# Kernel tuning notes

Hardware: AMD Instinct MI355X
Metric: run time of the kernel (lower is better)

Reference implementation:

```python
import jax, jax.numpy as jnp
import numpy as np
import math


def _neighbor_stack(x):
    # x: [b, nc, w, d] -> [b, nc, 3, w, d] with zero-padded prev/next chunks
    prev = jnp.pad(x[:, :-1], ((0, 0), (1, 0), (0, 0), (0, 0)))
    nxt = jnp.pad(x[:, 1:], ((0, 0), (0, 1), (0, 0), (0, 0)))
    return jnp.stack([prev, x, nxt], axis=2)


def local_attention(q, kv, Wq, Wkv, Wo, w):
    b, L, d_model = q.shape
    d_head = Wkv.shape[1] // 2
    h = d_model // d_head
    nc = L // w

    qp = (q @ Wq).reshape(b, L, h, d_head) / math.sqrt(d_head)
    kvp = kv @ Wkv  # [b, L, 2*d_head], single shared KV head (MQA)
    k, v = kvp[..., :d_head], kvp[..., d_head:]

    cq = qp.reshape(b, nc, w, h, d_head)
    k3 = _neighbor_stack(k.reshape(b, nc, w, d_head))  # [b, nc, 3, w, d]
    v3 = _neighbor_stack(v.reshape(b, nc, w, d_head))  # [b, nc, 3, w, d]

    # scores over (prev, self, next) chunks; padded edge chunks contribute
    # zero scores (exp(0)=1 in softmax), exactly as the torch F.pad(value=0) does.
    scores = jnp.einsum('bcxhd,bcpyd->bcxhpy', cq, k3)  # [b,nc,w,h,3,w]
    probs = jax.nn.softmax(scores.reshape(b, nc, w, h, 3 * w), axis=-1)
    probs = probs.reshape(b, nc, w, h, 3, w)

    ctx = jnp.einsum('bcxhpy,bcpyd->bcxhd', probs, v3)  # [b,nc,w,h,d]
    ctx = ctx.reshape(b, L, d_model)
    return ctx @ Wo


def setup_inputs() -> dict:
    key = jax.random.key(0)
    k1, k2, k3, k4, k5 = jax.random.split(key, 5)
    b, L, d_model, n_head = 1, 4096, 1024, 16
    d_head = d_model // n_head
    scale = 0.02
    return {
        'q': jax.random.normal(k1, (b, L, d_model), dtype=jnp.float32),
        'kv': jax.random.normal(k2, (b, L, d_model), dtype=jnp.float32),
        'Wq': jax.random.normal(k3, (d_model, d_model), dtype=jnp.float32) * scale,
        'Wkv': jax.random.normal(k4, (d_model, 2 * d_head), dtype=jnp.float32) * scale,
        'Wo': jax.random.normal(k5, (d_model, d_model), dtype=jnp.float32) * scale,
        'w': 512,
    }


def reference(q, kv, Wq, Wkv, Wo, w):
    return local_attention(q, kv, Wq, Wkv, Wo, w)
```

## Files before the change

kernel.cpp:

```cpp
#include <hip/hip_runtime.h>
#include <hip/hip_bf16.h>

typedef unsigned short u16;
typedef unsigned int u32;
typedef __attribute__((ext_vector_type(8))) short bf16x8;
typedef __attribute__((ext_vector_type(4))) float f32x4;
typedef __attribute__((ext_vector_type(16))) float f32x16;
typedef __attribute__((ext_vector_type(4))) u32 u32x4;

__device__ __forceinline__ u16 f2bf(float x) {
  __hip_bfloat16 h = __float2bfloat16(x);
  return __builtin_bit_cast(u16, h);
}

__device__ __forceinline__ u32 cvtpk(float lo, float hi) {
  u32 d;
  asm("v_cvt_pk_bf16_f32 %0, %1, %2" : "=v"(d) : "v"(lo), "v"(hi));
  return d;
}

#if __has_builtin(__builtin_amdgcn_exp2f)
#define EXP2(x) __builtin_amdgcn_exp2f(x)
#else
#define EXP2(x) __expf((x) * 0.6931471805599453f)
#endif

__device__ __forceinline__ bf16x8 mk_frag(u32 a, u32 b, u32 c, u32 d) {
  u32x4 v = {a, b, c, d};
  return __builtin_bit_cast(bf16x8, v);
}

__device__ __forceinline__ f32x16 mfma32(bf16x8 a, bf16x8 b, f32x16 c) {
  return __builtin_amdgcn_mfma_f32_32x32x16_bf16(a, b, c, 0, 0, 0);
}

__device__ __forceinline__ void gload16(const void* g, void* lds) {
  __builtin_amdgcn_global_load_lds((const __attribute__((address_space(1))) void*)g,
                                   (__attribute__((address_space(3))) void*)lds, 16, 0, 0);
}

__device__ __forceinline__ int xcd_swz(int bid, int cpx) {
  return (bid & 7) * cpx + (bid >> 3);
}

__global__ __launch_bounds__(256) void cvt_tw(const float* __restrict__ q, const float* __restrict__ kv,
                                              const float* __restrict__ Wq, const float* __restrict__ Wkv,
                                              const float* __restrict__ Wo, u16* __restrict__ qkbf,
                                              u16* __restrict__ wqt, u16* __restrict__ wkvt,
                                              u16* __restrict__ wot) {
  __shared__ float T[64][65];
  const int t = threadIdx.x;
  const int bid = blockIdx.x;
  if (bid < 4096) {
    int idx = bid * 256 + t;
    const float* src = (idx < 524288) ? q : kv;
    int li = idx & 524287;
    const float4* p = (const float4*)src + (size_t)li * 2;
    float4 a = p[0], b = p[1];
    bf16x8 vv;
    vv[0] = (short)f2bf(a.x); vv[1] = (short)f2bf(a.y);
    vv[2] = (short)f2bf(a.z); vv[3] = (short)f2bf(a.w);
    vv[4] = (short)f2bf(b.x); vv[5] = (short)f2bf(b.y);
    vv[6] = (short)f2bf(b.z); vv[7] = (short)f2bf(b.w);
    *(bf16x8*)(qkbf + (size_t)idx * 8) = vv;
    return;
  }
  const int wb = bid - 4096;
  const float* W; u16* Wt; int N, bx, by;
  if (wb < 256)      { W = Wq;  Wt = wqt;  N = 1024; bx = wb & 15; by = wb >> 4; }
  else if (wb < 512) { int b = wb - 256; W = Wo;  Wt = wot;  N = 1024; bx = b & 15; by = b >> 4; }
  else               { int b = wb - 512; W = Wkv; Wt = wkvt; N = 128;  bx = b & 1;  by = b >> 1; }
  const int K = 1024;
  const int n0 = bx * 64, k0 = by * 64;
  #pragma unroll
  for (int pass = 0; pass < 4; ++pass) {
    int r = pass * 16 + (t >> 4);
    int c = (t & 15) * 4;
    float4 v = *(const float4*)(W + (size_t)(k0 + r) * N + n0 + c);
    T[r][c] = v.x; T[r][c + 1] = v.y; T[r][c + 2] = v.z; T[r][c + 3] = v.w;
  }
  __syncthreads();
  #pragma unroll
  for (int s = 0; s < 2; ++s) {
    int n = s * 32 + (t >> 3);
    int kk = (t & 7) * 8;
    bf16x8 vv;
    #pragma unroll
    for (int i = 0; i < 8; ++i) vv[i] = (short)f2bf(T[kk + i][n]);
    *(bf16x8*)(Wt + (size_t)(n0 + n) * K + k0 + kk) = vv;
  }
}

template<int BF16OUT>
__global__ __launch_bounds__(256, 3) void gemm_bt(const u16* __restrict__ A, const u16* __restrict__ Bt,
                                                  void* __restrict__ Cout, int N, int K, float scale) {
  __shared__ __attribute__((aligned(16))) u16 As[128 * 128];
  __shared__ __attribute__((aligned(16))) u16 Bs[64 * 128];
  const int t = threadIdx.x;
  const int lane = t & 63, wv = t >> 6;
  const int g = lane >> 4, i16 = lane & 15;
  const int id = xcd_swz(blockIdx.x, 64);
  const int m0 = (id >> 4) * 128, n0 = (id & 15) * 64;
  const int wr = wv >> 1, wc = wv & 1;
  f32x4 acc[4][2] = {};
  for (int kt = 0; kt < K; kt += 128) {
    #pragma unroll
    for (int j = 0; j < 8; ++j) {
      int p = j * 4096 + t * 16;
      int row = p >> 8;
      int lg = (p & 255) ^ ((row & 15) << 4);
      gload16(A + (size_t)(m0 + row) * K + kt + (lg >> 1), (char*)As + p);
    }
    #pragma unroll
    for (int j = 0; j < 4; ++j) {
      int p = j * 4096 + t * 16;
      int row = p >> 8;
      int lg = (p & 255) ^ ((row & 15) << 4);
      gload16(Bt + (size_t)(n0 + row) * K + kt + (lg >> 1), (char*)Bs + p);
    }
    __syncthreads();
    bf16x8 af[4][4], bfr[4][2];
    #pragma unroll
    for (int kf = 0; kf < 4; ++kf) {
      #pragma unroll
      for (int x = 0; x < 4; ++x) {
        int ra = wr * 64 + x * 16 + i16;
        af[kf][x] = *(const bf16x8*)((const char*)As + ((ra * 256 + kf * 64 + g * 16) ^ ((ra & 15) << 4)));
      }
      #pragma unroll
      for (int x = 0; x < 2; ++x) {
        int rb = wc * 32 + x * 16 + i16;
        bfr[kf][x] = *(const bf16x8*)((const char*)Bs + ((rb * 256 + kf * 64 + g * 16) ^ ((rb & 15) << 4)));
      }
    }
    #pragma unroll
    for (int kf = 0; kf < 4; ++kf)
      #pragma unroll
      for (int mi = 0; mi < 4; ++mi)
        #pragma unroll
        for (int ni = 0; ni < 2; ++ni)
          acc[mi][ni] = __builtin_amdgcn_mfma_f32_16x16x32_bf16(af[kf][mi], bfr[kf][ni], acc[mi][ni], 0, 0, 0);
    __syncthreads();
  }
  #pragma unroll
  for (int mi = 0; mi < 4; ++mi)
    #pragma unroll
    for (int ni = 0; ni < 2; ++ni)
      #pragma unroll
      for (int r = 0; r < 4; ++r) {
        size_t off = (size_t)(m0 + wr * 64 + mi * 16 + g * 4 + r) * N + (n0 + wc * 32 + ni * 16 + i16);
        float v = acc[mi][ni][r] * scale;
        if (BF16OUT) ((u16*)Cout)[off] = f2bf(v);
        else ((float*)Cout)[off] = v;
      }
}

__global__ __launch_bounds__(256, 3) void gemm_qkv(const u16* __restrict__ qbf, const u16* __restrict__ kvbf,
                                                   const u16* __restrict__ wqt, const u16* __restrict__ wkvt,
                                                   u16* __restrict__ qp, u16* __restrict__ kvp,
                                                   u16* __restrict__ vtg) {
  __shared__ __attribute__((aligned(16))) u16 As[128 * 128];
  __shared__ __attribute__((aligned(16))) u16 Bs[64 * 128];
  const int t = threadIdx.x;
  const int lane = t & 63, wv = t >> 6;
  const int g = lane >> 4, i16 = lane & 15;
  const int wr = wv >> 1, wc = wv & 1;
  const int K = 1024;
  const int id = xcd_swz(blockIdx.x, 72);
  const bool iskv = id >= 512;
  const u16* A; const u16* Bt; int m0, n0;
  if (!iskv) { A = qbf;  Bt = wqt;  m0 = (id >> 4) * 128; n0 = (id & 15) * 64; }
  else       { int b = id - 512; A = kvbf; Bt = wkvt; m0 = (b >> 1) * 128; n0 = (b & 1) * 64; }
  f32x4 acc[4][2] = {};
  for (int kt = 0; kt < K; kt += 128) {
    #pragma unroll
    for (int j = 0; j < 8; ++j) {
      int p = j * 4096 + t * 16;
      int row = p >> 8;
      int lg = (p & 255) ^ ((row & 15) << 4);
      gload16(A + (size_t)(m0 + row) * K + kt + (lg >> 1), (char*)As + p);
    }
    #pragma unroll
    for (int j = 0; j < 4; ++j) {
      int p = j * 4096 + t * 16;
      int row = p >> 8;
      int lg = (p & 255) ^ ((row & 15) << 4);
      gload16(Bt + (size_t)(n0 + row) * K + kt + (lg >> 1), (char*)Bs + p);
    }
    __syncthreads();
    bf16x8 af[4][4], bfr[4][2];
    #pragma unroll
    for (int kf = 0; kf < 4; ++kf) {
      #pragma unroll
      for (int x = 0; x < 4; ++x) {
        int ra = wr * 64 + x * 16 + i16;
        af[kf][x] = *(const bf16x8*)((const char*)As + ((ra * 256 + kf * 64 + g * 16) ^ ((ra & 15) << 4)));
      }
      #pragma unroll
      for (int x = 0; x < 2; ++x) {
        int rb = wc * 32 + x * 16 + i16;
        bfr[kf][x] = *(const bf16x8*)((const char*)Bs + ((rb * 256 + kf * 64 + g * 16) ^ ((rb & 15) << 4)));
      }
    }
    #pragma unroll
    for (int kf = 0; kf < 4; ++kf)
      #pragma unroll
      for (int mi = 0; mi < 4; ++mi)
        #pragma unroll
        for (int ni = 0; ni < 2; ++ni)
          acc[mi][ni] = __builtin_amdgcn_mfma_f32_16x16x32_bf16(af[kf][mi], bfr[kf][ni], acc[mi][ni], 0, 0, 0);
    __syncthreads();
  }
  if (!iskv) {
    #pragma unroll
    for (int mi = 0; mi < 4; ++mi)
      #pragma unroll
      for (int ni = 0; ni < 2; ++ni)
        #pragma unroll
        for (int r = 0; r < 4; ++r)
          qp[(size_t)(m0 + wr * 64 + mi * 16 + g * 4 + r) * 1024 + n0 + wc * 32 + ni * 16 + i16] =
              f2bf(acc[mi][ni][r] * 0.18033688011112042f);
  } else if (n0 == 0) {
    #pragma unroll
    for (int mi = 0; mi < 4; ++mi)
      #pragma unroll
      for (int ni = 0; ni < 2; ++ni)
        #pragma unroll
        for (int r = 0; r < 4; ++r)
          kvp[(size_t)(m0 + wr * 64 + mi * 16 + g * 4 + r) * 64 + wc * 32 + ni * 16 + i16] =
              f2bf(acc[mi][ni][r]);
  } else {
    u16* CT = (u16*)As;
    #pragma unroll
    for (int mi = 0; mi < 4; ++mi)
      #pragma unroll
      for (int ni = 0; ni < 2; ++ni)
        #pragma unroll
        for (int r = 0; r < 4; ++r)
          CT[(wc * 32 + ni * 16 + i16) * 128 + wr * 64 + mi * 16 + g * 4 + r] = f2bf(acc[mi][ni][r]);
    __syncthreads();
    int d = t >> 2, c4 = t & 3;
    const u16* src = CT + d * 128 + c4 * 32;
    u16* dst = vtg + (size_t)d * 4096 + m0 + c4 * 32;
    #pragma unroll
    for (int j = 0; j < 4; ++j)
      *(bf16x8*)(dst + j * 8) = *(const bf16x8*)(src + j * 8);
  }
}

__global__ __launch_bounds__(256, 2) void attn_kernel(const u16* __restrict__ qp, const u16* __restrict__ kvp,
                                                      const u16* __restrict__ vtg, u16* __restrict__ ctx) {
  __shared__ __attribute__((aligned(16))) u16 Ks[2][2][64 * 64];
  __shared__ __attribute__((aligned(16))) u16 Vs[2][2][64 * 64];
  const int t = threadIdx.x;
  const int lane = t & 63, wv = t >> 6;
  const int g2 = wv >> 1, wq = wv & 1;
  const int tg = t & 127;
  const int hh = lane >> 5, q32 = lane & 31;
  const int id = xcd_swz(blockIdx.x, 64);
  const int qt = id & 3, hd = (id >> 2) & 15, c = id >> 6;
  const int q0 = c * 512 + qt * 128 + wq * 64;
  const int pk32 = (q32 & 19) | ((q32 & 4) << 1) | ((q32 & 8) >> 1);

  bf16x8 qfA[4], qfB[4];
  #pragma unroll
  for (int dt = 0; dt < 4; ++dt) {
    qfA[dt] = *(const bf16x8*)(qp + (size_t)(q0 + q32) * 1024 + hd * 64 + dt * 16 + hh * 8);
    qfB[dt] = *(const bf16x8*)(qp + (size_t)(q0 + 32 + q32) * 1024 + hd * 64 + dt * 16 + hh * 8);
  }

  const int kb0 = (c - 1) * 512;
  const int v0 = (c == 0) ? 8 : 0;
  const int nv = (c == 0 || c == 7) ? 16 : 24;
  const int n2 = nv >> 1;
  const int s0 = v0 + g2 * n2;
  const float lpad = g2 ? 0.f : 32.f * (float)(24 - nv);
  float lA = lpad, lB = lpad;
  f32x16 accA[2] = {}, accB[2] = {};

  int kA[4], vA[4];
  #pragma unroll
  for (int j = 0; j < 4; ++j) {
    int p = j * 2048 + tg * 16;
    int row = p >> 7;
    int lg = (p & 127) ^ ((row & 7) << 4);
    kA[j] = row * 64 + (lg >> 1);
    vA[j] = row * 4096 + (lg >> 1);
  }

  auto stage = [&](int b, int tile) {
    const int kb = kb0 + tile * 64;
    #pragma unroll
    for (int j = 0; j < 4; ++j)
      gload16(kvp + (size_t)(kb * 64 + kA[j]), (char*)Ks[g2][b] + j * 2048 + tg * 16);
    #pragma unroll
    for (int j = 0; j < 4; ++j)
      gload16(vtg + (size_t)(kb + vA[j]), (char*)Vs[g2][b] + j * 2048 + tg * 16);
  };

  stage(0, s0);

  for (int i = 0; i < n2; ++i) {
    asm volatile("s_waitcnt vmcnt(0)" ::: "memory");
    __builtin_amdgcn_s_barrier();
    if (i + 1 < n2) stage((i + 1) & 1, s0 + i + 1);
    const char* kbase0 = (const char*)Ks[g2][i & 1];
    const char* vbase0 = (const char*)Vs[g2][i & 1];
    f32x16 sA[2] = {}, sB[2] = {};
    #pragma unroll
    for (int kt = 0; kt < 2; ++kt) {
      const char* kbase = kbase0 + kt * 4096 + pk32 * 128;
      int kswz = (pk32 & 7) << 4;
      #pragma unroll
      for (int dt = 0; dt < 4; ++dt) {
        bf16x8 kf = *(const bf16x8*)(kbase + ((dt * 32 + hh * 16) ^ kswz));
        sA[kt] = mfma32(kf, qfA[dt], sA[kt]);
        sB[kt] = mfma32(kf, qfB[dt], sB[kt]);
      }
    }
    #pragma unroll
    for (int kt = 0; kt < 2; ++kt) {
      #pragma unroll
      for (int r = 0; r < 16; ++r) sA[kt][r] = EXP2(sA[kt][r]);
      #pragma unroll
      for (int r = 0; r < 16; ++r) sB[kt][r] = EXP2(sB[kt][r]);
      lA += (((sA[kt][0] + sA[kt][1]) + (sA[kt][2] + sA[kt][3])) + ((sA[kt][4] + sA[kt][5]) + (sA[kt][6] + sA[kt][7]))) +
            (((sA[kt][8] + sA[kt][9]) + (sA[kt][10] + sA[kt][11])) + ((sA[kt][12] + sA[kt][13]) + (sA[kt][14] + sA[kt][15])));
      lB += (((sB[kt][0] + sB[kt][1]) + (sB[kt][2] + sB[kt][3])) + ((sB[kt][4] + sB[kt][5]) + (sB[kt][6] + sB[kt][7]))) +
            (((sB[kt][8] + sB[kt][9]) + (sB[kt][10] + sB[kt][11])) + ((sB[kt][12] + sB[kt][13]) + (sB[kt][14] + sB[kt][15])));
      u32 wA[8], wB[8];
      #pragma unroll
      for (int j = 0; j < 8; ++j) wA[j] = cvtpk(sA[kt][2 * j], sA[kt][2 * j + 1]);
      #pragma unroll
      for (int j = 0; j < 8; ++j) wB[j] = cvtpk(sB[kt][2 * j], sB[kt][2 * j + 1]);
      bf16x8 pbA0 = mk_frag(wA[0], wA[1], wA[2], wA[3]);
      bf16x8 pbA1 = mk_frag(wA[4], wA[5], wA[6], wA[7]);
      bf16x8 pbB0 = mk_frag(wB[0], wB[1], wB[2], wB[3]);
      bf16x8 pbB1 = mk_frag(wB[4], wB[5], wB[6], wB[7]);
      int vswz = (q32 & 7) << 4;
      #pragma unroll
      for (int dtv = 0; dtv < 2; ++dtv) {
        const char* vbase = vbase0 + dtv * 4096 + q32 * 128;
        bf16x8 va0 = *(const bf16x8*)(vbase + ((kt * 64 + hh * 16) ^ vswz));
        accA[dtv] = mfma32(va0, pbA0, accA[dtv]);
        accB[dtv] = mfma32(va0, pbB0, accB[dtv]);
        bf16x8 va1 = *(const bf16x8*)(vbase + ((kt * 64 + 32 + hh * 16) ^ vswz));
        accA[dtv] = mfma32(va1, pbA1, accA[dtv]);
        accB[dtv] = mfma32(va1, pbB1, accB[dtv]);
      }
    }
  }

  __syncthreads();
  char* M = (char*)&Ks[0][0][0];
  float* Lx = (float*)((char*)&Vs[0][0][0] + 24576);
  if (g2 == 1) {
    #pragma unroll
    for (int set = 0; set < 2; ++set) {
      const f32x16* ac = set ? accB : accA;
      #pragma unroll
      for (int dtv = 0; dtv < 2; ++dtv)
        #pragma unroll
        for (int j = 0; j < 4; ++j) {
          f32x4 chunk = {ac[dtv][4 * j], ac[dtv][4 * j + 1], ac[dtv][4 * j + 2], ac[dtv][4 * j + 3]};
          int byte = lane * 128 + dtv * 64 + j * 16;
          *(f32x4*)(M + wq * 16384 + set * 8192 + (byte ^ ((lane & 7) << 4))) = chunk;
        }
      Lx[(wq * 2 + set) * 64 + lane] = set ? lB : lA;
    }
  }
  __syncthreads();
  if (g2 == 0) {
    #pragma unroll
    for (int set = 0; set < 2; ++set) {
      f32x16* ac = set ? accB : accA;
      #pragma unroll
      for (int dtv = 0; dtv < 2; ++dtv)
        #pragma unroll
        for (int j = 0; j < 4; ++j) {
          int byte = lane * 128 + dtv * 64 + j * 16;
          f32x4 chunk = *(const f32x4*)(M + wq * 16384 + set * 8192 + (byte ^ ((lane & 7) << 4)));
          #pragma unroll
          for (int e = 0; e < 4; ++e) ac[dtv][4 * j + e] += chunk[e];
        }
      float l = (set ? lB : lA) + Lx[(wq * 2 + set) * 64 + lane];
      l += __shfl_xor(l, 32);
      float rl = 1.0f / l;
      char* Ow = (char*)&Vs[0][0][0] + wq * 4096;
      #pragma unroll
      for (int dtv = 0; dtv < 2; ++dtv)
        #pragma unroll
        for (int j = 0; j < 4; ++j) {
          int d = dtv * 32 + 8 * j + 4 * hh;
          uint2 wp;
          wp.x = cvtpk(ac[dtv][4 * j] * rl, ac[dtv][4 * j + 1] * rl);
          wp.y = cvtpk(ac[dtv][4 * j + 2] * rl, ac[dtv][4 * j + 3] * rl);
          *(uint2*)(Ow + q32 * 128 + ((d * 2) ^ ((q32 & 7) << 4))) = wp;
        }
      asm volatile("s_waitcnt lgkmcnt(0)" ::: "memory");
      __builtin_amdgcn_sched_barrier(0);
      #pragma unroll
      for (int rep = 0; rep < 4; ++rep) {
        int q = lane >> 1, dblk = (lane & 1) * 4 + rep, d0 = dblk * 8;
        bf16x8 ov = *(const bf16x8*)(Ow + q * 128 + ((d0 * 2) ^ ((q & 7) << 4)));
        *(bf16x8*)(ctx + (size_t)(q0 + set * 32 + q) * 1024 + hd * 64 + d0) = ov;
      }
      asm volatile("s_waitcnt lgkmcnt(0) vmcnt(0)" ::: "memory");
      __builtin_amdgcn_sched_barrier(0);
    }
  }
}

extern "C" void kernel_launch(void* const* d_in, const int* in_sizes, int n_in,
                              void* d_out, int out_size, void* d_ws, size_t ws_size,
                              hipStream_t stream) {
  const float* q   = (const float*)d_in[0];
  const float* kv  = (const float*)d_in[1];
  const float* Wq  = (const float*)d_in[2];
  const float* Wkv = (const float*)d_in[3];
  const float* Wo  = (const float*)d_in[4];
  char* ws = (char*)d_ws;
  u16* qbf  = (u16*)(ws);
  u16* ctx  = (u16*)(ws);
  u16* kvbf = (u16*)(ws + 8388608);
  u16* qp   = (u16*)(ws + 16777216);
  u16* kvp  = (u16*)(ws + 25165824);
  u16* vtg  = (u16*)(ws + 25690112);
  u16* wqt  = (u16*)(ws + 26214400);
  u16* wkvt = (u16*)(ws + 28311552);
  u16* wot  = (u16*)(ws + 28573696);
  cvt_tw<<<4640, 256, 0, stream>>>(q, kv, Wq, Wkv, Wo, qbf, wqt, wkvt, wot);
  gemm_qkv<<<576, 256, 0, stream>>>(qbf, kvbf, wqt, wkvt, qp, kvp, vtg);
  attn_kernel<<<512, 256, 0, stream>>>(qp, kvp, vtg, ctx);
  gemm_bt<0><<<512, 256, 0, stream>>>(ctx, wot, (float*)d_out, 1024, 1024, 1.0f);
}
```

Before: 81.96 us.

## Double-buffer LDS tiles with BK=64 in projection GEMMs to overlap loads

Both GEMM kernels (gemm_bt and gemm_qkv) switch from a single 128-deep K tile to two 64-deep LDS buffers. The next tile's global-to-LDS loads are issued while MFMAs run on the current buffer, so a single wait plus barrier per iteration replaces the old load-sync-compute-sync sequence. Load offsets are precomputed once and the swizzle is adjusted for the 128-byte row pitch. Total LDS use stays the same, but each iteration does half as much compute between barriers, and the wait on all outstanding loads may leave little real overlap.

```diff
diff --git a/kernel.cpp b/kernel.cpp
--- a/kernel.cpp
+++ b/kernel.cpp
@@ -94,53 +94,67 @@
 template<int BF16OUT>
 __global__ __launch_bounds__(256, 3) void gemm_bt(const u16* __restrict__ A, const u16* __restrict__ Bt,
                                                   void* __restrict__ Cout, int N, int K, float scale) {
-  __shared__ __attribute__((aligned(16))) u16 As[128 * 128];
-  __shared__ __attribute__((aligned(16))) u16 Bs[64 * 128];
+  __shared__ __attribute__((aligned(16))) u16 As[2][128 * 64];
+  __shared__ __attribute__((aligned(16))) u16 Bs[2][64 * 64];
   const int t = threadIdx.x;
   const int lane = t & 63, wv = t >> 6;
   const int g = lane >> 4, i16 = lane & 15;
   const int id = xcd_swz(blockIdx.x, 64);
   const int m0 = (id >> 4) * 128, n0 = (id & 15) * 64;
   const int wr = wv >> 1, wc = wv & 1;
+  int aO[4], bO[2];
+  #pragma unroll
+  for (int j = 0; j < 4; ++j) {
+    int p = j * 4096 + t * 16;
+    int row = p >> 7;
+    int lg = (p & 127) ^ ((row & 7) << 4);
+    aO[j] = (m0 + row) * K + (lg >> 1);
+  }
+  #pragma unroll
+  for (int j = 0; j < 2; ++j) {
+    int p = j * 4096 + t * 16;
+    int row = p >> 7;
+    int lg = (p & 127) ^ ((row & 7) << 4);
+    bO[j] = (n0 + row) * K + (lg >> 1);
+  }
+  auto stage = [&](int b, int kt) {
+    #pragma unroll
+    for (int j = 0; j < 4; ++j)
+      gload16(A + (size_t)(aO[j] + kt), (char*)As[b] + j * 4096 + t * 16);
+    #pragma unroll
+    for (int j = 0; j < 2; ++j)
+      gload16(Bt + (size_t)(bO[j] + kt), (char*)Bs[b] + j * 4096 + t * 16);
+  };
   f32x4 acc[4][2] = {};
-  for (int kt = 0; kt < K; kt += 128) {
-    #pragma unroll
-    for (int j = 0; j < 8; ++j) {
-      int p = j * 4096 + t * 16;
-      int row = p >> 8;
-      int lg = (p & 255) ^ ((row & 15) << 4);
-      gload16(A + (size_t)(m0 + row) * K + kt + (lg >> 1), (char*)As + p);
-    }
-    #pragma unroll
-    for (int j = 0; j < 4; ++j) {
-      int p = j * 4096 + t * 16;
-      int row = p >> 8;
-      int lg = (p & 255) ^ ((row & 15) << 4);
-      gload16(Bt + (size_t)(n0 + row) * K + kt + (lg >> 1), (char*)Bs + p);
-    }
-    __syncthreads();
-    bf16x8 af[4][4], bfr[4][2];
-    #pragma unroll
-    for (int kf = 0; kf < 4; ++kf) {
+  const int NT = K >> 6;
+  stage(0, 0);
+  for (int it = 0; it < NT; ++it) {
+    asm volatile("s_waitcnt vmcnt(0)" ::: "memory");
+    __builtin_amdgcn_s_barrier();
+    if (it + 1 < NT) stage((it + 1) & 1, (it + 1) << 6);
+    const char* Ab = (const char*)As[it & 1];
+    const char* Bb = (const char*)Bs[it & 1];
+    bf16x8 af[2][4], bfr[2][2];
+    #pragma unroll
+    for (int kf = 0; kf < 2; ++kf) {
       #pragma unroll
       for (int x = 0; x < 4; ++x) {
         int ra = wr * 64 + x * 16 + i16;
-        af[kf][x] = *(const bf16x8*)((const char*)As + ((ra * 256 + kf * 64 + g * 16) ^ ((ra & 15) << 4)));
+        af[kf][x] = *(const bf16x8*)(Ab + ((ra * 128 + kf * 64 + g * 16) ^ ((ra & 7) << 4)));
       }
       #pragma unroll
       for (int x = 0; x < 2; ++x) {
         int rb = wc * 32 + x * 16 + i16;
-        bfr[kf][x] = *(const bf16x8*)((const char*)Bs + ((rb * 256 + kf * 64 + g * 16) ^ ((rb & 15) << 4)));
-      }
-    }
-    #pragma unroll
-    for (int kf = 0; kf < 4; ++kf)
+        bfr[kf][x] = *(const bf16x8*)(Bb + ((rb * 128 + kf * 64 + g * 16) ^ ((rb & 7) << 4)));
+      }
+    }
+    #pragma unroll
+    for (int kf = 0; kf < 2; ++kf)
       #pragma unroll
       for (int mi = 0; mi < 4; ++mi)
         #pragma unroll
         for (int ni = 0; ni < 2; ++ni)
           acc[mi][ni] = __builtin_amdgcn_mfma_f32_16x16x32_bf16(af[kf][mi], bfr[kf][ni], acc[mi][ni], 0, 0, 0);
-    __syncthreads();
   }
   #pragma unroll
   for (int mi = 0; mi < 4; ++mi)
@@ -159,8 +173,8 @@
                                                    const u16* __restrict__ wqt, const u16* __restrict__ wkvt,
                                                    u16* __restrict__ qp, u16* __restrict__ kvp,
                                                    u16* __restrict__ vtg) {
-  __shared__ __attribute__((aligned(16))) u16 As[128 * 128];
-  __shared__ __attribute__((aligned(16))) u16 Bs[64 * 128];
+  __shared__ __attribute__((aligned(16))) u16 As[2][128 * 64];
+  __shared__ __attribute__((aligned(16))) u16 Bs[2][64 * 64];
   const int t = threadIdx.x;
   const int lane = t & 63, wv = t >> 6;
   const int g = lane >> 4, i16 = lane & 15;
@@ -171,45 +185,59 @@
   const u16* A; const u16* Bt; int m0, n0;
   if (!iskv) { A = qbf;  Bt = wqt;  m0 = (id >> 4) * 128; n0 = (id & 15) * 64; }
   else       { int b = id - 512; A = kvbf; Bt = wkvt; m0 = (b >> 1) * 128; n0 = (b & 1) * 64; }
+  int aO[4], bO[2];
+  #pragma unroll
+  for (int j = 0; j < 4; ++j) {
+    int p = j * 4096 + t * 16;
+    int row = p >> 7;
+    int lg = (p & 127) ^ ((row & 7) << 4);
+    aO[j] = (m0 + row) * K + (lg >> 1);
+  }
+  #pragma unroll
+  for (int j = 0; j < 2; ++j) {
+    int p = j * 4096 + t * 16;
+    int row = p >> 7;
+    int lg = (p & 127) ^ ((row & 7) << 4);
+    bO[j] = (n0 + row) * K + (lg >> 1);
+  }
+  auto stage = [&](int b, int kt) {
+    #pragma unroll
+    for (int j = 0; j < 4; ++j)
+      gload16(A + (size_t)(aO[j] + kt), (char*)As[b] + j * 4096 + t * 16);
+    #pragma unroll
+    for (int j = 0; j < 2; ++j)
+      gload16(Bt + (size_t)(bO[j] + kt), (char*)Bs[b] + j * 4096 + t * 16);
+  };
   f32x4 acc[4][2] = {};
-  for (int kt = 0; kt < K; kt += 128) {
-    #pragma unroll
-    for (int j = 0; j < 8; ++j) {
-      int p = j * 4096 + t * 16;
-      int row = p >> 8;
-      int lg = (p & 255) ^ ((row & 15) << 4);
-      gload16(A + (size_t)(m0 + row) * K + kt + (lg >> 1), (char*)As + p);
-    }
-    #pragma unroll
-    for (int j = 0; j < 4; ++j) {
-      int p = j * 4096 + t * 16;
-      int row = p >> 8;
-      int lg = (p & 255) ^ ((row & 15) << 4);
-      gload16(Bt + (size_t)(n0 + row) * K + kt + (lg >> 1), (char*)Bs + p);
-    }
-    __syncthreads();
-    bf16x8 af[4][4], bfr[4][2];
-    #pragma unroll
-    for (int kf = 0; kf < 4; ++kf) {
+  const int NT = 16;
+  stage(0, 0);
+  for (int it = 0; it < NT; ++it) {
+    asm volatile("s_waitcnt vmcnt(0)" ::: "memory");
+    __builtin_amdgcn_s_barrier();
+    if (it + 1 < NT) stage((it + 1) & 1, (it + 1) << 6);
+    const char* Ab = (const char*)As[it & 1];
+    const char* Bb = (const char*)Bs[it & 1];
+    bf16x8 af[2][4], bfr[2][2];
+    #pragma unroll
+    for (int kf = 0; kf < 2; ++kf) {
       #pragma unroll
       for (int x = 0; x < 4; ++x) {
         int ra = wr * 64 + x * 16 + i16;
-        af[kf][x] = *(const bf16x8*)((const char*)As + ((ra * 256 + kf * 64 + g * 16) ^ ((ra & 15) << 4)));
+        af[kf][x] = *(const bf16x8*)(Ab + ((ra * 128 + kf * 64 + g * 16) ^ ((ra & 7) << 4)));
       }
       #pragma unroll
       for (int x = 0; x < 2; ++x) {
         int rb = wc * 32 + x * 16 + i16;
-        bfr[kf][x] = *(const bf16x8*)((const char*)Bs + ((rb * 256 + kf * 64 + g * 16) ^ ((rb & 15) << 4)));
-      }
-    }
-    #pragma unroll
-    for (int kf = 0; kf < 4; ++kf)
+        bfr[kf][x] = *(const bf16x8*)(Bb + ((rb * 128 + kf * 64 + g * 16) ^ ((rb & 7) << 4)));
+      }
+    }
+    #pragma unroll
+    for (int kf = 0; kf < 2; ++kf)
       #pragma unroll
       for (int mi = 0; mi < 4; ++mi)
         #pragma unroll
         for (int ni = 0; ni < 2; ++ni)
           acc[mi][ni] = __builtin_amdgcn_mfma_f32_16x16x32_bf16(af[kf][mi], bfr[kf][ni], acc[mi][ni], 0, 0, 0);
-    __syncthreads();
   }
   if (!iskv) {
     #pragma unroll
@@ -230,7 +258,8 @@
           kvp[(size_t)(m0 + wr * 64 + mi * 16 + g * 4 + r) * 64 + wc * 32 + ni * 16 + i16] =
               f2bf(acc[mi][ni][r]);
   } else {
-    u16* CT = (u16*)As;
+    __syncthreads();
+    u16* CT = (u16*)&As[0][0];
     #pragma unroll
     for (int mi = 0; mi < 4; ++mi)
       #pragma unroll
```

New measurement: 84.96 us. 1.04x slower.
